# Optimization experiments

Hardware: AMD Instinct MI355X
Metric: run time of the kernel (lower is better)

## Reference

```python
import jax, jax.numpy as jnp
import numpy as np

B, N, F, D, DB, C = 1024, 65536, 64, 512, 1024, 96


def _ln(x, g, b):
    m = x.mean(-1, keepdims=True)
    v = ((x - m) ** 2).mean(-1, keepdims=True)
    return (x - m) * jax.lax.rsqrt(v + 1e-5) * g + b


def setup_inputs() -> dict:
    key = jax.random.key(0)
    ks = jax.random.split(key, 16)
    rn = lambda k, shape, s=1.0: jax.random.normal(k, shape, dtype=jnp.float32) * s
    s_in, s_d, s_db = 1.0 / np.sqrt(F), 1.0 / np.sqrt(D), 1.0 / np.sqrt(DB)
    bound = 1.0 / np.sqrt(2.0)
    return {
        "x_num": rn(ks[0], (B, F)),
        "candidate_num": rn(ks[1], (N, F)),
        "candidate_y": rn(ks[2], (N,)),
        "lin_W": rn(ks[3], (F, D), s_in), "lin_b": jnp.zeros((D,), jnp.float32),
        "e_W1": rn(ks[4], (D, DB), s_d), "e_b1": jnp.zeros((DB,), jnp.float32),
        "e_W2": rn(ks[5], (DB, D), s_db), "e_b2": jnp.zeros((D,), jnp.float32),
        "mix_g": jnp.ones((D,), jnp.float32), "mix_b": jnp.zeros((D,), jnp.float32),
        "K_W": rn(ks[6], (D, D), s_d), "K_b": jnp.zeros((D,), jnp.float32),
        "lab_W": rn(ks[7], (1, D), bound), "lab_b": rn(ks[8], (D,), bound),
        "T_W1": rn(ks[9], (D, DB), s_d), "T_b1": jnp.zeros((DB,), jnp.float32),
        "T_W2": rn(ks[10], (DB, D), s_db),
        "p_ln_g": jnp.ones((D,), jnp.float32), "p_ln_b": jnp.zeros((D,), jnp.float32),
        "p_W1": rn(ks[11], (D, DB), s_d), "p_b1": jnp.zeros((DB,), jnp.float32),
        "p_W2": rn(ks[12], (DB, D), s_db), "p_b2": jnp.zeros((D,), jnp.float32),
        "h_ln_g": jnp.ones((D,), jnp.float32), "h_ln_b": jnp.zeros((D,), jnp.float32),
        "h_W": rn(ks[13], (D, 1), s_d), "h_b": jnp.zeros((1,), jnp.float32),
        "context_size": C,
    }


def reference(x_num, candidate_num, candidate_y,
              lin_W, lin_b, e_W1, e_b1, e_W2, e_b2, mix_g, mix_b, K_W, K_b,
              lab_W, lab_b, T_W1, T_b1, T_W2,
              p_ln_g, p_ln_b, p_W1, p_b1, p_W2, p_b2,
              h_ln_g, h_ln_b, h_W, h_b, context_size):
    def encode(z):
        h = z @ lin_W + lin_b
        h = h + jax.nn.relu(h @ e_W1 + e_b1) @ e_W2 + e_b2  # residual encoder block
        k = _ln(h, mix_g, mix_b) @ K_W + K_b                 # mixer-norm + K projection
        return h, k

    _, cand_k = encode(candidate_num)   # [N, D]
    x, k = encode(x_num)                # [B, D]

    # faiss IndexFlatL2: squared-L2 k-NN over candidate keys -> [B, N] then top-k
    d2 = (k * k).sum(-1, keepdims=True) - 2.0 * (k @ cand_k.T) + (cand_k * cand_k).sum(-1)
    _, idx = jax.lax.top_k(-d2, context_size)   # [B, C] nearest candidates

    ctx_k = cand_k[idx]          # [B, C, D] irregular gather
    ctx_y = candidate_y[idx]     # [B, C]

    # similarities = -||k - k_i||^2, recomputed from gathered keys as in source
    sims = -((k * k).sum(-1, keepdims=True)
             - 2.0 * jnp.einsum('bd,bcd->bc', k, ctx_k)
             + (ctx_k * ctx_k).sum(-1))
    probs = jax.nn.softmax(sims, axis=-1)  # context_dropout=0 (eval)

    y_emb = ctx_y[..., None] @ lab_W + lab_b            # label_encoder_: Linear(1, D)
    diff = k[:, None, :] - ctx_k                        # [B, C, D]
    values = y_emb + jax.nn.relu(diff @ T_W1 + T_b1) @ T_W2
    ctx_x = jnp.einsum('bc,bcd->bd', probs, values)

    x = x + ctx_x
    x = x + jax.nn.relu(_ln(x, p_ln_g, p_ln_b) @ p_W1 + p_b1) @ p_W2 + p_b2  # predictor block
    return jax.nn.relu(_ln(x, h_ln_g, h_ln_b)) @ h_W + h_b                   # head -> [B, 1]
```

## Files before the change

kernel.cpp:

```cpp
#include <hip/hip_runtime.h>

#define NB   1024
#define NN   65536
#define NF   64
#define ND   512
#define NDB  1024
#define NC   96

#define BB_C 256
#define BB_D 128

#define TK_SPLIT 16
#define TK_SEG   (NN / TK_SPLIT)
#define TK_CAND  (TK_SPLIT * NC)

typedef unsigned short ushort;
typedef __attribute__((ext_vector_type(8))) short short8;
typedef __attribute__((ext_vector_type(4))) float floatx4;

__device__ __forceinline__ ushort f2bf(float f) {
    unsigned u = __float_as_uint(f);
    u += 0x7fffu + ((u >> 16) & 1u);
    return (ushort)(u >> 16);
}
__device__ __forceinline__ float bf2f(ushort h) {
    return __uint_as_float(((unsigned)h) << 16);
}
__device__ __forceinline__ int lds_off(int m, int c) {
    return m * 32 + (((c + (m >> 1)) & 3) << 3);
}

__device__ __forceinline__ void gload16(const ushort* g, ushort* l)
{
    void* gv = (void*)g;
    void* lv = (void*)l;
    __builtin_amdgcn_global_load_lds(
        (__attribute__((address_space(1))) void*)gv,
        (__attribute__((address_space(3))) void*)lv, 16, 0, 0);
}

__device__ __forceinline__ void xcd_slab(int& bx, int& by)
{
    const int gx  = gridDim.x;
    const int nwg = gx * gridDim.y;
    int x = blockIdx.x, y = blockIdx.y;
    if (!(nwg & 7)) {
        const int wg = y * gx + x;
        const int t  = (wg & 7) * (nwg >> 3) + (wg >> 3);
        x = t % gx; y = t / gx;
    }
    bx = x; by = y;
}

__global__ __launch_bounds__(256) void gemm_ss(
    const ushort* __restrict__ Ah_g, const ushort* __restrict__ Al_g,
    const ushort* __restrict__ Bh_g, const ushort* __restrict__ Bl_g,
    const float* __restrict__ scoresq, float* __restrict__ Sf,
    int M, int N, int K)
{
    __shared__ ushort Ah[128 * 32], Al[128 * 32];
    __shared__ ushort Bh[128 * 32], Bl[128 * 32];
    const int tid = threadIdx.x;
    const int lane = tid & 63, wid = tid >> 6;
    const int wm = (wid & 1) * 64, wn = (wid >> 1) * 64;
    const int lane15 = lane & 15, quad = lane >> 4;
    const int row0 = blockIdx.y * 128, col0 = blockIdx.x * 128;

    const int srow = tid >> 2;
    const int scl  = tid & 3;
    const int cp   = (scl - (srow >> 1)) & 3;
    const size_t ga0 = (size_t)(row0 + srow) * K + cp * 8;
    const size_t ga1 = (size_t)(row0 + 64 + srow) * K + cp * 8;
    const size_t gb0 = (size_t)(col0 + srow) * K + cp * 8;
    const size_t gb1 = (size_t)(col0 + 64 + srow) * K + cp * 8;
    const int l0 = tid * 8;
    const int l1 = 2048 + tid * 8;

    floatx4 acc[4][4];
#pragma unroll
    for (int i = 0; i < 4; i++)
#pragma unroll
        for (int j = 0; j < 4; j++) acc[i][j] = (floatx4){0.f, 0.f, 0.f, 0.f};

    for (int k0 = 0; k0 < K; k0 += 32) {
        __syncthreads();
        gload16(Ah_g + ga0 + k0, Ah + l0);
        gload16(Ah_g + ga1 + k0, Ah + l1);
        gload16(Al_g + ga0 + k0, Al + l0);
        gload16(Al_g + ga1 + k0, Al + l1);
        gload16(Bh_g + gb0 + k0, Bh + l0);
        gload16(Bh_g + gb1 + k0, Bh + l1);
        gload16(Bl_g + gb0 + k0, Bl + l0);
        gload16(Bl_g + gb1 + k0, Bl + l1);
        __syncthreads();

        short8 ah[4], al[4], bh[4], bl[4];
#pragma unroll
        for (int t = 0; t < 4; t++) {
            const int am = wm + t * 16 + lane15;
            const int bn = wn + t * 16 + lane15;
            ah[t] = *(const short8*)(Ah + lds_off(am, quad));
            al[t] = *(const short8*)(Al + lds_off(am, quad));
            bh[t] = *(const short8*)(Bh + lds_off(bn, quad));
            bl[t] = *(const short8*)(Bl + lds_off(bn, quad));
        }
#pragma unroll
        for (int i = 0; i < 4; i++)
#pragma unroll
            for (int j = 0; j < 4; j++) {
                acc[i][j] = __builtin_amdgcn_mfma_f32_16x16x32_bf16(ah[i], bh[j], acc[i][j], 0, 0, 0);
                acc[i][j] = __builtin_amdgcn_mfma_f32_16x16x32_bf16(ah[i], bl[j], acc[i][j], 0, 0, 0);
                acc[i][j] = __builtin_amdgcn_mfma_f32_16x16x32_bf16(al[i], bh[j], acc[i][j], 0, 0, 0);
            }
    }

#pragma unroll
    for (int i = 0; i < 4; i++)
#pragma unroll
        for (int j = 0; j < 4; j++) {
            const int gc = col0 + wn + j * 16 + lane15;
            const int rb = row0 + wm + i * 16 + quad * 4;
            const float sv = scoresq[gc];
#pragma unroll
            for (int r = 0; r < 4; r++) {
                const size_t o = (size_t)(rb + r) * N + gc;
                Sf[o] = sv - 2.f * acc[i][j][r];
            }
        }
}

__global__ __launch_bounds__(256) void gemm_ss_n64(
    const ushort* __restrict__ Ah_g, const ushort* __restrict__ Al_g,
    const ushort* __restrict__ Bh_g, const ushort* __restrict__ Bl_g,
    const float* __restrict__ bias,
    const ushort* __restrict__ resh, const ushort* __restrict__ resl,
    ushort* __restrict__ Ch, ushort* __restrict__ Cl,
    int M, int N, int K, int relu)
{
    __shared__ ushort Ah[128 * 64], Al[128 * 64];
    __shared__ ushort Bh[64 * 64], Bl[64 * 64];
    const int tid = threadIdx.x;
    const int lane = tid & 63, wid = tid >> 6;
    const int wm = wid * 32;
    const int lane15 = lane & 15, quad = lane >> 4;
    int bx, by; xcd_slab(bx, by);
    const int row0 = by * 128, col0 = bx * 64;

    const int srow = tid >> 2;
    const int scl  = tid & 3;
    const int cp   = (scl - (srow >> 1)) & 3;
    const size_t ga0 = (size_t)(row0 + srow) * K + cp * 8;
    const size_t ga1 = (size_t)(row0 + 64 + srow) * K + cp * 8;
    const size_t gb  = (size_t)(col0 + srow) * K + cp * 8;
    const int l0 = tid * 8;
    const int l1 = 2048 + tid * 8;

    floatx4 acc[2][4];
#pragma unroll
    for (int i = 0; i < 2; i++)
#pragma unroll
        for (int j = 0; j < 4; j++) acc[i][j] = (floatx4){0.f, 0.f, 0.f, 0.f};

    for (int k0 = 0; k0 < K; k0 += 64) {
        __syncthreads();
        gload16(Ah_g + ga0 + k0,      Ah + l0);
        gload16(Ah_g + ga1 + k0,      Ah + l1);
        gload16(Ah_g + ga0 + k0 + 32, Ah + 4096 + l0);
        gload16(Ah_g + ga1 + k0 + 32, Ah + 4096 + l1);
        gload16(Al_g + ga0 + k0,      Al + l0);
        gload16(Al_g + ga1 + k0,      Al + l1);
        gload16(Al_g + ga0 + k0 + 32, Al + 4096 + l0);
        gload16(Al_g + ga1 + k0 + 32, Al + 4096 + l1);
        gload16(Bh_g + gb + k0,       Bh + l0);
        gload16(Bh_g + gb + k0 + 32,  Bh + 2048 + l0);
        gload16(Bl_g + gb + k0,       Bl + l0);
        gload16(Bl_g + gb + k0 + 32,  Bl + 2048 + l0);
        __syncthreads();

#pragma unroll
        for (int kk = 0; kk < 2; kk++) {
            const int ao = kk * 4096, bo = kk * 2048;
            short8 ah[2], al[2], bh[4], bl[4];
#pragma unroll
            for (int t = 0; t < 2; t++) {
                const int am = wm + t * 16 + lane15;
                ah[t] = *(const short8*)(Ah + ao + lds_off(am, quad));
                al[t] = *(const short8*)(Al + ao + lds_off(am, quad));
            }
#pragma unroll
            for (int j = 0; j < 4; j++) {
                const int bn = j * 16 + lane15;
                bh[j] = *(const short8*)(Bh + bo + lds_off(bn, quad));
                bl[j] = *(const short8*)(Bl + bo + lds_off(bn, quad));
            }
#pragma unroll
            for (int i = 0; i < 2; i++)
#pragma unroll
                for (int j = 0; j < 4; j++) {
                    acc[i][j] = __builtin_amdgcn_mfma_f32_16x16x32_bf16(ah[i], bh[j], acc[i][j], 0, 0, 0);
                    acc[i][j] = __builtin_amdgcn_mfma_f32_16x16x32_bf16(ah[i], bl[j], acc[i][j], 0, 0, 0);
                    acc[i][j] = __builtin_amdgcn_mfma_f32_16x16x32_bf16(al[i], bh[j], acc[i][j], 0, 0, 0);
                }
        }
    }

#pragma unroll
    for (int i = 0; i < 2; i++)
#pragma unroll
        for (int j = 0; j < 4; j++) {
            const int gc = col0 + j * 16 + lane15;
            const int rb = row0 + wm + i * 16 + quad * 4;
            const float bv = bias ? bias[gc] : 0.f;
#pragma unroll
            for (int r = 0; r < 4; r++) {
                const size_t o = (size_t)(rb + r) * N + gc;
                float v = acc[i][j][r] + bv;
                if (resh) v += bf2f(resh[o]) + bf2f(resl[o]);
                if (relu) v = fmaxf(v, 0.f);
                ushort h = f2bf(v);
                Ch[o] = h;
                Cl[o] = f2bf(v - bf2f(h));
            }
        }
}

__global__ __launch_bounds__(256) void gemm_ss_small(
    const ushort* __restrict__ Ah_g, const ushort* __restrict__ Al_g,
    const ushort* __restrict__ Bh_g, const ushort* __restrict__ Bl_g,
    const float* __restrict__ bias,
    const ushort* resh, const ushort* resl,
    const float* resf,
    ushort* Ch, ushort* Cl,
    float* outf,
    int M, int N, int K, int relu)
{
    __shared__ ushort Ah[64 * 64], Al[64 * 64];
    __shared__ ushort Bh[64 * 64], Bl[64 * 64];
    const int tid = threadIdx.x;
    const int lane = tid & 63, wid = tid >> 6;
    const int wm = (wid & 1) * 32, wn = (wid >> 1) * 32;
    const int lane15 = lane & 15, quad = lane >> 4;
    int bx, by; xcd_slab(bx, by);
    const int row0 = by * 64, col0 = bx * 64;

    const int srow = tid >> 2;
    const int scl  = tid & 3;
    const int cp   = (scl - (srow >> 1)) & 3;
    const size_t ga = (size_t)(row0 + srow) * K + cp * 8;
    const size_t gb = (size_t)(col0 + srow) * K + cp * 8;
    const int l = tid * 8;

    floatx4 acc[2][2];
#pragma unroll
    for (int i = 0; i < 2; i++)
#pragma unroll
        for (int j = 0; j < 2; j++) acc[i][j] = (floatx4){0.f, 0.f, 0.f, 0.f};

    for (int k0 = 0; k0 < K; k0 += 64) {
        __syncthreads();
        gload16(Ah_g + ga + k0,      Ah + l);
        gload16(Ah_g + ga + k0 + 32, Ah + 2048 + l);
        gload16(Al_g + ga + k0,      Al + l);
        gload16(Al_g + ga + k0 + 32, Al + 2048 + l);
        gload16(Bh_g + gb + k0,      Bh + l);
        gload16(Bh_g + gb + k0 + 32, Bh + 2048 + l);
        gload16(Bl_g + gb + k0,      Bl + l);
        gload16(Bl_g + gb + k0 + 32, Bl + 2048 + l);
        __syncthreads();

#pragma unroll
        for (int kk = 0; kk < 2; kk++) {
            const int so = kk * 2048;
            short8 ah[2], al[2], bh[2], bl[2];
#pragma unroll
            for (int t = 0; t < 2; t++) {
                const int am = wm + t * 16 + lane15;
                const int bn = wn + t * 16 + lane15;
                ah[t] = *(const short8*)(Ah + so + lds_off(am, quad));
                al[t] = *(const short8*)(Al + so + lds_off(am, quad));
                bh[t] = *(const short8*)(Bh + so + lds_off(bn, quad));
                bl[t] = *(const short8*)(Bl + so + lds_off(bn, quad));
            }
#pragma unroll
            for (int i = 0; i < 2; i++)
#pragma unroll
                for (int j = 0; j < 2; j++) {
                    acc[i][j] = __builtin_amdgcn_mfma_f32_16x16x32_bf16(ah[i], bh[j], acc[i][j], 0, 0, 0);
                    acc[i][j] = __builtin_amdgcn_mfma_f32_16x16x32_bf16(ah[i], bl[j], acc[i][j], 0, 0, 0);
                    acc[i][j] = __builtin_amdgcn_mfma_f32_16x16x32_bf16(al[i], bh[j], acc[i][j], 0, 0, 0);
                }
        }
    }

#pragma unroll
    for (int i = 0; i < 2; i++)
#pragma unroll
        for (int j = 0; j < 2; j++) {
            const int gc = col0 + wn + j * 16 + lane15;
            const int rb = row0 + wm + i * 16 + quad * 4;
            const float bv = bias ? bias[gc] : 0.f;
#pragma unroll
            for (int r = 0; r < 4; r++) {
                const size_t o = (size_t)(rb + r) * N + gc;
                float v = acc[i][j][r] + bv;
                if (resh) v += bf2f(resh[o]) + bf2f(resl[o]);
                if (resf) v += resf[o];
                if (relu) v = fmaxf(v, 0.f);
                if (outf) outf[o] = v;
                if (Ch) {
                    ushort h = f2bf(v);
                    Ch[o] = h;
                    Cl[o] = f2bf(v - bf2f(h));
                }
            }
        }
}

__global__ __launch_bounds__(256) void diff_pl_kernel(
    const ushort* __restrict__ kxh, const ushort* __restrict__ kxl,
    const ushort* __restrict__ ckh, const ushort* __restrict__ ckl,
    const int* __restrict__ idx,
    ushort* __restrict__ DD, int Mrows)
{
    const int g = blockIdx.x * 256 + threadIdx.x;
    if (g >= Mrows * (ND / 8)) return;
    const int r  = g >> 6;
    const int d  = (g & 63) * 8;
    const int b_loc = r / NC;
    const int ci = idx[r];
    const size_t xb = (size_t)b_loc * ND + d;
    const size_t cb = (size_t)ci * ND + d;

    short8 xh = *(const short8*)(kxh + xb);
    short8 xl = *(const short8*)(kxl + xb);
    short8 ch = *(const short8*)(ckh + cb);
    short8 cl = *(const short8*)(ckl + cb);
    short8 dd;
#pragma unroll
    for (int i = 0; i < 8; i++) {
        const float a = bf2f((ushort)xh[i]) + bf2f((ushort)xl[i]);
        const float c = bf2f((ushort)ch[i]) + bf2f((ushort)cl[i]);
        dd[i] = (short)f2bf(a - c);
    }
    *(short8*)(DD + (size_t)r * ND + d) = dd;
}

__global__ __launch_bounds__(256) void gemm_bf16_n64(
    const ushort* __restrict__ A, const ushort* __restrict__ BTh,
    const float* __restrict__ bias,
    ushort* __restrict__ Cbf, float* __restrict__ Cf,
    int M, int N, int K, int relu)
{
    __shared__ ushort Ah[128 * 64];
    __shared__ ushort Bh[64 * 64];
    const int tid = threadIdx.x;
    const int lane = tid & 63, wid = tid >> 6;
    const int wm = wid * 32;
    const int lane15 = lane & 15, quad = lane >> 4;
    int bx, by; xcd_slab(bx, by);
    const int row0 = by * 128, col0 = bx * 64;

    const int srow = tid >> 2;
    const int scl  = tid & 3;
    const int cp   = (scl - (srow >> 1)) & 3;
    const size_t ga0 = (size_t)(row0 + srow) * K + cp * 8;
    const size_t ga1 = (size_t)(row0 + 64 + srow) * K + cp * 8;
    const size_t gb  = (size_t)(col0 + srow) * K + cp * 8;
    const int l0 = tid * 8, l1 = 2048 + tid * 8;

    floatx4 acc[2][4];
#pragma unroll
    for (int i = 0; i < 2; i++)
#pragma unroll
        for (int j = 0; j < 4; j++) acc[i][j] = (floatx4){0.f, 0.f, 0.f, 0.f};

    for (int k0 = 0; k0 < K; k0 += 64) {
        __syncthreads();
        gload16(A + ga0 + k0,      Ah + l0);
        gload16(A + ga1 + k0,      Ah + l1);
        gload16(A + ga0 + k0 + 32, Ah + 4096 + l0);
        gload16(A + ga1 + k0 + 32, Ah + 4096 + l1);
        gload16(BTh + gb + k0,      Bh + l0);
        gload16(BTh + gb + k0 + 32, Bh + 2048 + l0);
        __syncthreads();

#pragma unroll
        for (int kk = 0; kk < 2; kk++) {
            const int ao = kk * 4096, bo = kk * 2048;
            short8 ah[2], bh[4];
#pragma unroll
            for (int t = 0; t < 2; t++)
                ah[t] = *(const short8*)(Ah + ao + lds_off(wm + t * 16 + lane15, quad));
#pragma unroll
            for (int j = 0; j < 4; j++)
                bh[j] = *(const short8*)(Bh + bo + lds_off(j * 16 + lane15, quad));
#pragma unroll
            for (int i = 0; i < 2; i++)
#pragma unroll
                for (int j = 0; j < 4; j++)
                    acc[i][j] = __builtin_amdgcn_mfma_f32_16x16x32_bf16(ah[i], bh[j], acc[i][j], 0, 0, 0);
        }
    }

#pragma unroll
    for (int i = 0; i < 2; i++)
#pragma unroll
        for (int j = 0; j < 4; j++) {
            const int gc = col0 + j * 16 + lane15;
            const int rb = row0 + wm + i * 16 + quad * 4;
            const float bv = bias ? bias[gc] : 0.f;
#pragma unroll
            for (int rr = 0; rr < 4; rr++) {
                const size_t o = (size_t)(rb + rr) * N + gc;
                float v = acc[i][j][rr] + bv;
                if (relu) v = fmaxf(v, 0.f);
                if (Cbf) Cbf[o] = f2bf(v);
                if (Cf)  Cf[o] = v;
            }
        }
}

__global__ __launch_bounds__(256) void split_wt_kernel(
    const float* __restrict__ W, ushort* __restrict__ WTh,
    ushort* __restrict__ WTl, int K, int N)
{
    const int o = blockIdx.x * 256 + threadIdx.x;
    if (o < K * N) {
        const int n = o / K, k = o - n * K;
        const float x = W[(size_t)k * N + n];
        const ushort h = f2bf(x);
        WTh[o] = h;
        WTl[o] = f2bf(x - bf2f(h));
    }
}

__global__ __launch_bounds__(256) void split_pl_kernel(
    const float* __restrict__ X, ushort* __restrict__ Xh,
    ushort* __restrict__ Xl, int n)
{
    const int i = blockIdx.x * 256 + threadIdx.x;
    if (i < n) {
        const float x = X[i];
        const ushort h = f2bf(x);
        Xh[i] = h;
        Xl[i] = f2bf(x - bf2f(h));
    }
}

__global__ __launch_bounds__(256) void ln_kernel(
    const float* __restrict__ X, const float* __restrict__ g,
    const float* __restrict__ b, float* __restrict__ Y, int relu)
{
    const int lane = threadIdx.x & 63;
    const int row  = blockIdx.x * 4 + (threadIdx.x >> 6);
    const float* x = X + (size_t)row * ND;
    const int d = lane * 8;

    float4 v0 = *(const float4*)(x + d);
    float4 v1 = *(const float4*)(x + d + 4);
    float s = v0.x + v0.y + v0.z + v0.w + v1.x + v1.y + v1.z + v1.w;
    float q = v0.x*v0.x + v0.y*v0.y + v0.z*v0.z + v0.w*v0.w
            + v1.x*v1.x + v1.y*v1.y + v1.z*v1.z + v1.w*v1.w;
#pragma unroll
    for (int off = 32; off; off >>= 1) {
        s += __shfl_down(s, off);
        q += __shfl_down(q, off);
    }
    s = __shfl(s, 0); q = __shfl(q, 0);
    const float mean = s * (1.f / ND);
    const float var  = q * (1.f / ND) - mean * mean;
    const float rs   = rsqrtf(var + 1e-5f);

    float4 g0 = *(const float4*)(g + d);
    float4 g1 = *(const float4*)(g + d + 4);
    float4 b0 = *(const float4*)(b + d);
    float4 b1 = *(const float4*)(b + d + 4);
    float4 o0, o1;
    o0.x = (v0.x - mean) * rs * g0.x + b0.x;
    o0.y = (v0.y - mean) * rs * g0.y + b0.y;
    o0.z = (v0.z - mean) * rs * g0.z + b0.z;
    o0.w = (v0.w - mean) * rs * g0.w + b0.w;
    o1.x = (v1.x - mean) * rs * g1.x + b1.x;
    o1.y = (v1.y - mean) * rs * g1.y + b1.y;
    o1.z = (v1.z - mean) * rs * g1.z + b1.z;
    o1.w = (v1.w - mean) * rs * g1.w + b1.w;
    if (relu) {
        o0.x = fmaxf(o0.x, 0.f); o0.y = fmaxf(o0.y, 0.f);
        o0.z = fmaxf(o0.z, 0.f); o0.w = fmaxf(o0.w, 0.f);
        o1.x = fmaxf(o1.x, 0.f); o1.y = fmaxf(o1.y, 0.f);
        o1.z = fmaxf(o1.z, 0.f); o1.w = fmaxf(o1.w, 0.f);
    }
    float* y = Y + (size_t)row * ND;
    *(float4*)(y + d)     = o0;
    *(float4*)(y + d + 4) = o1;
}

__global__ __launch_bounds__(256) void ln_pl_kernel(
    const ushort* __restrict__ Xh, const ushort* __restrict__ Xl,
    const float* __restrict__ g, const float* __restrict__ b,
    ushort* __restrict__ Yh, ushort* __restrict__ Yl)
{
    const int lane = threadIdx.x & 63;
    const int row  = blockIdx.x * 4 + (threadIdx.x >> 6);
    const int d = lane * 8;
    const size_t base = (size_t)row * ND + d;

    short8 xh = *(const short8*)(Xh + base);
    short8 xl = *(const short8*)(Xl + base);
    float v[8];
#pragma unroll
    for (int i = 0; i < 8; i++) v[i] = bf2f((ushort)xh[i]) + bf2f((ushort)xl[i]);

    float s = 0.f, q = 0.f;
#pragma unroll
    for (int i = 0; i < 8; i++) { s += v[i]; q += v[i] * v[i]; }
#pragma unroll
    for (int off = 32; off; off >>= 1) {
        s += __shfl_down(s, off);
        q += __shfl_down(q, off);
    }
    s = __shfl(s, 0); q = __shfl(q, 0);
    const float mean = s * (1.f / ND);
    const float var  = q * (1.f / ND) - mean * mean;
    const float rs   = rsqrtf(var + 1e-5f);

    short8 yh, yl;
#pragma unroll
    for (int i = 0; i < 8; i++) {
        const float o = (v[i] - mean) * rs * g[d + i] + b[d + i];
        const ushort h = f2bf(o);
        yh[i] = (short)h;
        yl[i] = (short)f2bf(o - bf2f(h));
    }
    *(short8*)(Yh + base) = yh;
    *(short8*)(Yl + base) = yl;
}

__global__ __launch_bounds__(256) void sqnorm_pl_kernel(
    const ushort* __restrict__ Xh, const ushort* __restrict__ Xl,
    float* __restrict__ sq)
{
    const int lane = threadIdx.x & 63;
    const int row  = blockIdx.x * 4 + (threadIdx.x >> 6);
    const size_t base = (size_t)row * ND + lane * 8;
    short8 xh = *(const short8*)(Xh + base);
    short8 xl = *(const short8*)(Xl + base);
    float q = 0.f;
#pragma unroll
    for (int i = 0; i < 8; i++) {
        float v = bf2f((ushort)xh[i]) + bf2f((ushort)xl[i]);
        q += v * v;
    }
#pragma unroll
    for (int off = 32; off; off >>= 1) q += __shfl_down(q, off);
    if (lane == 0) sq[row] = q;
}

__device__ __forceinline__ unsigned fkey(float f)
{
    unsigned u = __float_as_uint(f);
    return (u & 0x80000000u) ? ~u : (u | 0x80000000u);
}
__device__ __forceinline__ float inv_fkey(unsigned u)
{
    return __uint_as_float((u & 0x80000000u) ? (u & 0x7FFFFFFFu) : ~u);
}

struct SelState {
    unsigned lo;
    unsigned long long hi;
    int krem;
    int done;
    unsigned long long T;
    int need;
};

template <int KPT>
__device__ __forceinline__ void adaptive_select(
    const unsigned (&key)[KPT], unsigned* hist, unsigned* wtot,
    SelState* st, int tid, int kwant)
{
    const int lane = tid & 63, wid = tid >> 6;

    unsigned mn = 0xFFFFFFFFu, mx = 0u;
#pragma unroll
    for (int j = 0; j < KPT; j++) {
        mn = min(mn, key[j]);
        mx = max(mx, key[j]);
    }
#pragma unroll
    for (int off = 32; off; off >>= 1) {
        mn = min(mn, (unsigned)__shfl_down((int)mn, off));
        mx = max(mx, (unsigned)__shfl_down((int)mx, off));
    }
    if (lane == 0) { hist[wid] = mn; hist[8 + wid] = mx; }
    if (tid == 0) st->done = 0;
    __syncthreads();
    if (tid == 0) {
        unsigned gmn = min(min(hist[0], hist[1]), min(hist[2], hist[3]));
        unsigned gmx = max(max(hist[8], hist[9]), max(hist[10], hist[11]));
        st->lo = gmn;
        st->hi = (unsigned long long)gmx + 1ull;
        st->krem = kwant;
    }
    __syncthreads();

    for (int iter = 0; iter < 6 && !st->done; iter++) {
        const unsigned lo = st->lo;
        const unsigned long long hi = st->hi;
        const int krem = st->krem;
        const unsigned long long span = hi - lo;
        int shift = 0;
        if (span > 256ull) {
            const int nb = 64 - __builtin_clzll(span - 1ull);
            shift = nb - 8;
        }
        hist[tid] = 0u;
        __syncthreads();
#pragma unroll
        for (int j = 0; j < KPT; j++) {
            const unsigned u = key[j];
            if (u >= lo && (unsigned long long)u < hi)
                atomicAdd(&hist[(u - lo) >> shift], 1u);
        }
        __syncthreads();
        const unsigned c = hist[tid];
        unsigned v = c;
#pragma unroll
        for (int off = 1; off < 64; off <<= 1) {
            const unsigned t = (unsigned)__shfl_up((int)v, off);
            if (lane >= off) v += t;
        }
        if (lane == 63) wtot[wid] = v;
        __syncthreads();
        unsigned pre = 0;
        for (int w = 0; w < 3; w++) pre += (w < wid) ? wtot[w] : 0u;
        const int incl = (int)(v + pre);
        const int excl = incl - (int)c;
        if (excl < krem && incl >= krem) {
            const unsigned long long binlo =
                (unsigned long long)lo + ((unsigned long long)tid << shift);
            if (shift == 0) {
                st->T = binlo;
                st->need = krem - excl;
                st->done = 1;
            } else if (incl == krem) {
                st->T = binlo + (1ull << shift);
                st->need = 0;
                st->done = 1;
            } else {
                st->lo = (unsigned)binlo;
                const unsigned long long nhi = binlo + (1ull << shift);
                st->hi = nhi < hi ? nhi : hi;
                st->krem = krem - excl;
            }
        }
        __syncthreads();
    }
}

__global__ __launch_bounds__(256) void topk_seg(
    const float* __restrict__ S, unsigned* __restrict__ K1key,
    int* __restrict__ K1idx)
{
    const int r = blockIdx.y, seg = blockIdx.x;
    const float* p = S + (size_t)r * NN + seg * TK_SEG;
    __shared__ unsigned hist[256];
    __shared__ unsigned wtot[4];
    __shared__ SelState st;
    __shared__ int cA, cB;
    const int tid = threadIdx.x;

    unsigned key[16];
#pragma unroll
    for (int j = 0; j < 16; j++) key[j] = fkey(p[tid + j * 256]);

    if (tid == 0) { cA = 0; cB = 0; }
    adaptive_select<16>(key, hist, wtot, &st, tid, NC);

    const unsigned long long T = st.T;
    const int need = st.need;
    const int cntLess = NC - need;
    const size_t obase = ((size_t)r * TK_SPLIT + seg) * NC;
#pragma unroll
    for (int j = 0; j < 16; j++) {
        const unsigned u = key[j];
        if ((unsigned long long)u < T) {
            const int pos = atomicAdd(&cA, 1);
            K1key[obase + pos] = u;
            K1idx[obase + pos] = seg * TK_SEG + tid + j * 256;
        } else if ((unsigned long long)u == T) {
            const int pos = atomicAdd(&cB, 1);
            if (pos < need) {
                K1key[obase + cntLess + pos] = u;
                K1idx[obase + cntLess + pos] = seg * TK_SEG + tid + j * 256;
            }
        }
    }
}

__global__ __launch_bounds__(256) void topk_merge(
    const unsigned* __restrict__ K1key, const int* __restrict__ K1idx,
    int* __restrict__ idx_out, float* __restrict__ val_out, int b0)
{
    const int r = blockIdx.x;
    const int b = b0 + r;
    __shared__ unsigned hist[256];
    __shared__ unsigned wtot[4];
    __shared__ SelState st;
    __shared__ int cA, cB;
    const int tid = threadIdx.x;
    const size_t ibase = (size_t)r * TK_CAND;

    unsigned key[6];
    int      kidx[6];
#pragma unroll
    for (int j = 0; j < 6; j++) {
        key[j]  = K1key[ibase + tid + j * 256];
        kidx[j] = K1idx[ibase + tid + j * 256];
    }

    if (tid == 0) { cA = 0; cB = 0; }
    adaptive_select<6>(key, hist, wtot, &st, tid, NC);

    const unsigned long long T = st.T;
    const int need = st.need;
    const int cntLess = NC - need;
#pragma unroll
    for (int j = 0; j < 6; j++) {
        const unsigned u = key[j];
        if ((unsigned long long)u < T) {
            const int pos = atomicAdd(&cA, 1);
            idx_out[b * NC + pos] = kidx[j];
            val_out[b * NC + pos] = inv_fkey(u);
        } else if ((unsigned long long)u == T) {
            const int pos = atomicAdd(&cB, 1);
            if (pos < need) {
                idx_out[b * NC + cntLess + pos] = kidx[j];
                val_out[b * NC + cntLess + pos] = inv_fkey(u);
            }
        }
    }
}

__global__ __launch_bounds__(128) void probs_kernel(
    const float* __restrict__ svals, float* __restrict__ probs)
{
    const int b = blockIdx.x;
    const int tid = threadIdx.x;
    __shared__ float red[128];
    const bool valid = tid < NC;
    float s = valid ? -svals[b * NC + tid] : -3.4e38f;
    red[tid] = s;
    __syncthreads();
#pragma unroll
    for (int off = 64; off; off >>= 1) {
        if (tid < off) red[tid] = fmaxf(red[tid], red[tid + off]);
        __syncthreads();
    }
    const float m = red[0];
    __syncthreads();
    float e = valid ? expf(s - m) : 0.f;
    red[tid] = e;
    __syncthreads();
#pragma unroll
    for (int off = 64; off; off >>= 1) {
        if (tid < off) red[tid] += red[tid + off];
        __syncthreads();
    }
    const float sum = red[0];
    if (valid) probs[b * NC + tid] = e / sum;
}

__global__ __launch_bounds__(256) void ctx_kernel(
    const float* __restrict__ VAL, const float* __restrict__ probs,
    const float* __restrict__ cand_y, const int* __restrict__ idx,
    const float* __restrict__ labW, const float* __restrict__ labb,
    const ushort* __restrict__ xinh, const ushort* __restrict__ xinl,
    float* __restrict__ xout, int b0)
{
    const int b_loc = blockIdx.x;
    const int b = b0 + b_loc;
    const int tid = threadIdx.x;
    __shared__ float pv[NC];
    __shared__ float red[256];
    float py_part = 0.f;
    if (tid < NC) {
        float p = probs[b * NC + tid];
        pv[tid] = p;
        py_part = p * cand_y[idx[b * NC + tid]];
    }
    red[tid] = py_part;
    __syncthreads();
#pragma unroll
    for (int off = 128; off; off >>= 1) {
        if (tid < off) red[tid] += red[tid + off];
        __syncthreads();
    }
    const float py = red[0];

    for (int d = tid; d < ND; d += 256) {
        const float* vp = VAL + (size_t)b_loc * NC * ND + d;
        float acc = 0.f;
#pragma unroll 8
        for (int c = 0; c < NC; c++) acc += pv[c] * vp[(size_t)c * ND];
        float ctx = acc + py * labW[d] + labb[d];
        const size_t o = (size_t)b * ND + d;
        xout[o] = bf2f(xinh[o]) + bf2f(xinl[o]) + ctx;
    }
}

__global__ __launch_bounds__(64) void head_kernel(
    const float* __restrict__ X, const float* __restrict__ hW,
    const float* __restrict__ hb, float* __restrict__ out)
{
    const int b = blockIdx.x;
    const int lane = threadIdx.x;
    const float* x = X + (size_t)b * ND;
    float acc = 0.f;
#pragma unroll
    for (int j = 0; j < 8; j++) {
        int d = lane + 64 * j;
        acc += x[d] * hW[d];
    }
#pragma unroll
    for (int off = 32; off; off >>= 1) acc += __shfl_down(acc, off);
    if (lane == 0) out[b] = acc + hb[0];
}

extern "C" void kernel_launch(void* const* d_in, const int* in_sizes, int n_in,
                              void* d_out, int out_size, void* d_ws, size_t ws_size,
                              hipStream_t stream)
{
    const float* x_num    = (const float*)d_in[0];
    const float* cand_num = (const float*)d_in[1];
    const float* cand_y   = (const float*)d_in[2];
    const float* lin_W    = (const float*)d_in[3];
    const float* lin_b    = (const float*)d_in[4];
    const float* e_W1     = (const float*)d_in[5];
    const float* e_b1     = (const float*)d_in[6];
    const float* e_W2     = (const float*)d_in[7];
    const float* e_b2     = (const float*)d_in[8];
    const float* mix_g    = (const float*)d_in[9];
    const float* mix_b    = (const float*)d_in[10];
    const float* K_W      = (const float*)d_in[11];
    const float* K_b      = (const float*)d_in[12];
    const float* lab_W    = (const float*)d_in[13];
    const float* lab_b    = (const float*)d_in[14];
    const float* T_W1     = (const float*)d_in[15];
    const float* T_b1     = (const float*)d_in[16];
    const float* T_W2     = (const float*)d_in[17];
    const float* p_ln_g   = (const float*)d_in[18];
    const float* p_ln_b   = (const float*)d_in[19];
    const float* p_W1     = (const float*)d_in[20];
    const float* p_b1     = (const float*)d_in[21];
    const float* p_W2     = (const float*)d_in[22];
    const float* p_b2     = (const float*)d_in[23];
    const float* h_ln_g   = (const float*)d_in[24];
    const float* h_ln_b   = (const float*)d_in[25];
    const float* h_W      = (const float*)d_in[26];
    const float* h_b      = (const float*)d_in[27];
    float* out = (float*)d_out;
    (void)in_sizes; (void)n_in; (void)out_size;

    const int NTOT = NN + NB;

    size_t off = 0;
    auto ralloc = [&](size_t bytes) -> void* {
        void* p = (char*)d_ws + off;
        off += (bytes + 255) & ~(size_t)255;
        return p;
    };
    auto falloc = [&](size_t n) -> float*  { return (float*)ralloc(n * 4); };
    auto ualloc = [&](size_t n) -> ushort* { return (ushort*)ralloc(n * 2); };

    ushort* WP_lin_h = ualloc((size_t)ND * NF);
    ushort* WP_lin_l = ualloc((size_t)ND * NF);
    ushort* WP_e1_h  = ualloc((size_t)NDB * ND);
    ushort* WP_e1_l  = ualloc((size_t)NDB * ND);
    ushort* WP_e2_h  = ualloc((size_t)ND * NDB);
    ushort* WP_e2_l  = ualloc((size_t)ND * NDB);
    ushort* WP_kw_h  = ualloc((size_t)ND * ND);
    ushort* WP_kw_l  = ualloc((size_t)ND * ND);
    ushort* WP_t1_h  = ualloc((size_t)NDB * ND);
    ushort* WP_t1_l  = ualloc((size_t)NDB * ND);
    ushort* WP_t2_h  = ualloc((size_t)ND * NDB);
    ushort* WP_t2_l  = ualloc((size_t)ND * NDB);
    ushort* WP_p1_h  = ualloc((size_t)NDB * ND);
    ushort* WP_p1_l  = ualloc((size_t)NDB * ND);
    ushort* WP_p2_h  = ualloc((size_t)ND * NDB);
    ushort* WP_p2_l  = ualloc((size_t)ND * NDB);

    ushort* R_CKh = ualloc((size_t)NTOT * ND);
    ushort* R_CKl = ualloc((size_t)NTOT * ND);
    float*  R_sq  = falloc(NTOT);

    ushort* X2h = ualloc((size_t)NB * ND);
    ushort* X2l = ualloc((size_t)NB * ND);
    ushort* Lxh = ualloc((size_t)NB * ND);
    ushort* Lxl = ualloc((size_t)NB * ND);
    ushort* Tph = ualloc((size_t)NB * NDB);
    ushort* Tpl = ualloc((size_t)NB * NDB);

    int*    R_idx = (int*)ralloc((size_t)NB * NC * 4);
    float*  R_ssel= falloc((size_t)NB * NC);
    float*  R_prob= falloc((size_t)NB * NC);
    float*  R_xupd= falloc((size_t)NB * ND);
    float*  R_lnx = falloc((size_t)NB * ND);
    float*  R_x2  = falloc((size_t)NB * ND);
    float*  R_lnx2= falloc((size_t)NB * ND);
    unsigned* K1key = (unsigned*)ralloc((size_t)BB_C * TK_CAND * 4);
    int*      K1idx = (int*)ralloc((size_t)BB_C * TK_CAND * 4);

    int CH;
    {
        const size_t remain = (ws_size > off) ? (ws_size - off) : 0;
        CH = (remain >= (size_t)13312 * 6144 + (size_t)(4u << 20)) ? 13312 : 8320;
    }
    size_t scr_bytes = (size_t)CH * 6144;
    const size_t scores_bytes = (size_t)BB_C * NN * 4;
    const size_t values_bytes = (size_t)BB_D * NC * (ND*2 + NDB*2 + ND*4);
    if (scr_bytes < scores_bytes) scr_bytes = scores_bytes;
    if (scr_bytes < values_bytes) scr_bytes = values_bytes;
    char* SCR = (char*)ralloc(scr_bytes);

    auto sw = [&](const float* W, ushort* WTh, ushort* WTl, int K, int N) {
        split_wt_kernel<<<dim3((K * N + 255) / 256), dim3(256), 0, stream>>>(W, WTh, WTl, K, N);
    };
    sw(lin_W, WP_lin_h, WP_lin_l, NF, ND);
    sw(e_W1,  WP_e1_h,  WP_e1_l,  ND, NDB);
    sw(e_W2,  WP_e2_h,  WP_e2_l,  NDB, ND);
    sw(K_W,   WP_kw_h,  WP_kw_l,  ND, ND);
    sw(T_W1,  WP_t1_h,  WP_t1_l,  ND, NDB);
    sw(T_W2,  WP_t2_h,  WP_t2_l,  NDB, ND);
    sw(p_W1,  WP_p1_h,  WP_p1_l,  ND, NDB);
    sw(p_W2,  WP_p2_h,  WP_p2_l,  NDB, ND);

    auto gn64 = [&](const ushort* Ah, const ushort* Al, const ushort* Bh,
                    const ushort* Bl, const float* bias, const ushort* resh,
                    const ushort* resl, ushort* Ch, ushort* Cl,
                    int M, int Nn, int K, int relu) {
        gemm_ss_n64<<<dim3(Nn / 64, M / 128), dim3(256), 0, stream>>>(
            Ah, Al, Bh, Bl, bias, resh, resl, Ch, Cl, M, Nn, K, relu);
    };
    auto gsm = [&](const ushort* Ah, const ushort* Al, const ushort* Bh,
                   const ushort* Bl, const float* bias, const ushort* resh,
                   const ushort* resl, const float* resf, ushort* Ch,
                   ushort* Cl, float* outf, int M, int Nn, int K, int relu) {
        gemm_ss_small<<<dim3(Nn / 64, M / 64), dim3(256), 0, stream>>>(
            Ah, Al, Bh, Bl, bias, resh, resl, resf, Ch, Cl, outf, M, Nn, K, relu);
    };

    {
        ushort* Hh = (ushort*)SCR;
        ushort* Hl = Hh + (size_t)CH * ND;
        ushort* Th = Hl + (size_t)CH * ND;
        ushort* Tl = Th + (size_t)CH * NDB;
        ushort* CNh = Th;
        ushort* CNl = Tl;
        ushort* Gh  = Th;
        ushort* Gl  = Tl;

        for (int n0 = 0; n0 < NTOT; n0 += CH) {
            int candRows = NN - n0;
            if (candRows > CH) candRows = CH;
            if (candRows < 0)  candRows = 0;
            const int xRows = CH - candRows;

            if (candRows)
                split_pl_kernel<<<dim3((candRows * NF + 255) / 256), dim3(256), 0, stream>>>(
                    cand_num + (size_t)n0 * NF, CNh, CNl, candRows * NF);
            if (xRows)
                split_pl_kernel<<<dim3((xRows * NF + 255) / 256), dim3(256), 0, stream>>>(
                    x_num, CNh + (size_t)candRows * NF, CNl + (size_t)candRows * NF,
                    xRows * NF);

            gsm(CNh, CNl, WP_lin_h, WP_lin_l, lin_b, nullptr, nullptr, nullptr,
                Hh, Hl, nullptr, CH, ND, NF, 0);
            gn64(Hh, Hl, WP_e1_h, WP_e1_l, e_b1, nullptr, nullptr,
                 Th, Tl, CH, NDB, ND, 1);
            gsm(Th, Tl, WP_e2_h, WP_e2_l, e_b2, Hh, Hl, nullptr,
                Hh, Hl, nullptr, CH, ND, NDB, 0);

            if (xRows) {
                hipMemcpyAsync(X2h, Hh + (size_t)candRows * ND,
                               (size_t)NB * ND * 2, hipMemcpyDeviceToDevice, stream);
                hipMemcpyAsync(X2l, Hl + (size_t)candRows * ND,
                               (size_t)NB * ND * 2, hipMemcpyDeviceToDevice, stream);
            }

            ln_pl_kernel<<<dim3(CH / 4), dim3(256), 0, stream>>>(
                Hh, Hl, mix_g, mix_b, Gh, Gl);
            gsm(Gh, Gl, WP_kw_h, WP_kw_l, K_b, nullptr, nullptr, nullptr,
                R_CKh + (size_t)n0 * ND, R_CKl + (size_t)n0 * ND, nullptr,
                CH, ND, ND, 0);
            sqnorm_pl_kernel<<<dim3(CH / 4), dim3(256), 0, stream>>>(
                R_CKh + (size_t)n0 * ND, R_CKl + (size_t)n0 * ND, R_sq + n0);
        }
    }

    const ushort* kxh = R_CKh + (size_t)NN * ND;
    const ushort* kxl = R_CKl + (size_t)NN * ND;

    for (int b0 = 0; b0 < NB; b0 += BB_C) {
        float* S = (float*)SCR;
        gemm_ss<<<dim3(NN / 128, BB_C / 128), dim3(256), 0, stream>>>(
            kxh + (size_t)b0 * ND, kxl + (size_t)b0 * ND, R_CKh, R_CKl,
            R_sq, S, BB_C, NN, ND);
        topk_seg<<<dim3(TK_SPLIT, BB_C), dim3(256), 0, stream>>>(S, K1key, K1idx);
        topk_merge<<<dim3(BB_C), dim3(256), 0, stream>>>(K1key, K1idx,
                                                         R_idx, R_ssel, b0);
    }
    probs_kernel<<<dim3(NB), dim3(128), 0, stream>>>(R_ssel, R_prob);

    for (int b0 = 0; b0 < NB; b0 += BB_D) {
        const int M = BB_D * NC;
        ushort* DD  = (ushort*)SCR;
        ushort* TT  = DD + (size_t)M * ND;
        float*  VAL = (float*)(TT + (size_t)M * NDB);

        diff_pl_kernel<<<dim3((M * (ND / 8) + 255) / 256), dim3(256), 0, stream>>>(
            kxh + (size_t)b0 * ND, kxl + (size_t)b0 * ND,
            R_CKh, R_CKl, R_idx + b0 * NC, DD, M);
        gemm_bf16_n64<<<dim3(NDB / 64, M / 128), dim3(256), 0, stream>>>(
            DD, WP_t1_h, T_b1, TT, nullptr, M, NDB, ND, 1);
        gemm_bf16_n64<<<dim3(ND / 64, M / 128), dim3(256), 0, stream>>>(
            TT, WP_t2_h, nullptr, nullptr, VAL, M, ND, NDB, 0);
        ctx_kernel<<<dim3(BB_D), dim3(256), 0, stream>>>(
            VAL, R_prob, cand_y, R_idx, lab_W, lab_b, X2h, X2l, R_xupd, b0);
    }

    ln_kernel<<<dim3(NB / 4), dim3(256), 0, stream>>>(R_xupd, p_ln_g, p_ln_b, R_lnx, 0);
    split_pl_kernel<<<dim3((NB * ND + 255) / 256), dim3(256), 0, stream>>>(
        R_lnx, Lxh, Lxl, NB * ND);
    gsm(Lxh, Lxl, WP_p1_h, WP_p1_l, p_b1, nullptr, nullptr, nullptr,
        Tph, Tpl, nullptr, NB, NDB, ND, 1);
    gsm(Tph, Tpl, WP_p2_h, WP_p2_l, p_b2, nullptr, nullptr, R_xupd,
        nullptr, nullptr, R_x2, NB, ND, NDB, 0);
    ln_kernel<<<dim3(NB / 4), dim3(256), 0, stream>>>(R_x2, h_ln_g, h_ln_b, R_lnx2, 1);
    head_kernel<<<dim3(NB), dim3(64), 0, stream>>>(R_lnx2, h_W, h_b, out);
}
```

Baseline: 2.052 ms.

## Use 64-wide split GEMM for encoder, vectorize topk loads, split ctx grid

The encoder's lin, e_W2 and K projection GEMMs move from the gsm kernel to the 128x64-tile split-precision gn64 kernel. The restrict qualifiers are dropped from gn64's residual and output pointers so it can be called in place (residual aliases the output). topk_seg now reads scores as float4 with the element indices remapped to match, and ctx_kernel runs on a 2-D grid so each block handles half of the D columns. The aim is better occupancy or tiling for the encoder GEMMs and wider loads, at the cost of smaller tiles and possibly less reuse per block.

```diff
diff --git a/kernel.cpp b/kernel.cpp
--- a/kernel.cpp
+++ b/kernel.cpp
@@ -133,8 +133,8 @@
     const ushort* __restrict__ Ah_g, const ushort* __restrict__ Al_g,
     const ushort* __restrict__ Bh_g, const ushort* __restrict__ Bl_g,
     const float* __restrict__ bias,
-    const ushort* __restrict__ resh, const ushort* __restrict__ resl,
-    ushort* __restrict__ Ch, ushort* __restrict__ Cl,
+    const ushort* resh, const ushort* resl,
+    ushort* Ch, ushort* Cl,
     int M, int N, int K, int relu)
 {
     __shared__ ushort Ah[128 * 64], Al[128 * 64];
@@ -673,7 +673,13 @@
 
     unsigned key[16];
 #pragma unroll
-    for (int j = 0; j < 16; j++) key[j] = fkey(p[tid + j * 256]);
+    for (int j = 0; j < 4; j++) {
+        float4 v = *(const float4*)(p + tid * 4 + j * 1024);
+        key[j * 4 + 0] = fkey(v.x);
+        key[j * 4 + 1] = fkey(v.y);
+        key[j * 4 + 2] = fkey(v.z);
+        key[j * 4 + 3] = fkey(v.w);
+    }
 
     if (tid == 0) { cA = 0; cB = 0; }
     adaptive_select<16>(key, hist, wtot, &st, tid, NC);
@@ -685,15 +691,16 @@
 #pragma unroll
     for (int j = 0; j < 16; j++) {
         const unsigned u = key[j];
+        const int eidx = seg * TK_SEG + tid * 4 + (j >> 2) * 1024 + (j & 3);
         if ((unsigned long long)u < T) {
             const int pos = atomicAdd(&cA, 1);
             K1key[obase + pos] = u;
-            K1idx[obase + pos] = seg * TK_SEG + tid + j * 256;
+            K1idx[obase + pos] = eidx;
         } else if ((unsigned long long)u == T) {
             const int pos = atomicAdd(&cB, 1);
             if (pos < need) {
                 K1key[obase + cntLess + pos] = u;
-                K1idx[obase + cntLess + pos] = seg * TK_SEG + tid + j * 256;
+                K1idx[obase + cntLess + pos] = eidx;
             }
         }
     }
@@ -799,15 +806,14 @@
     }
     const float py = red[0];
 
-    for (int d = tid; d < ND; d += 256) {
-        const float* vp = VAL + (size_t)b_loc * NC * ND + d;
-        float acc = 0.f;
+    const int d = blockIdx.y * 256 + tid;
+    const float* vp = VAL + (size_t)b_loc * NC * ND + d;
+    float acc = 0.f;
 #pragma unroll 8
-        for (int c = 0; c < NC; c++) acc += pv[c] * vp[(size_t)c * ND];
-        float ctx = acc + py * labW[d] + labb[d];
-        const size_t o = (size_t)b * ND + d;
-        xout[o] = bf2f(xinh[o]) + bf2f(xinl[o]) + ctx;
-    }
+    for (int c = 0; c < NC; c++) acc += pv[c] * vp[(size_t)c * ND];
+    float ctx = acc + py * labW[d] + labb[d];
+    const size_t o = (size_t)b * ND + d;
+    xout[o] = bf2f(xinh[o]) + bf2f(xinl[o]) + ctx;
 }
 
 __global__ __launch_bounds__(64) void head_kernel(
@@ -975,12 +981,12 @@
                     x_num, CNh + (size_t)candRows * NF, CNl + (size_t)candRows * NF,
                     xRows * NF);
 
-            gsm(CNh, CNl, WP_lin_h, WP_lin_l, lin_b, nullptr, nullptr, nullptr,
-                Hh, Hl, nullptr, CH, ND, NF, 0);
+            gn64(CNh, CNl, WP_lin_h, WP_lin_l, lin_b, nullptr, nullptr,
+                 Hh, Hl, CH, ND, NF, 0);
             gn64(Hh, Hl, WP_e1_h, WP_e1_l, e_b1, nullptr, nullptr,
                  Th, Tl, CH, NDB, ND, 1);
-            gsm(Th, Tl, WP_e2_h, WP_e2_l, e_b2, Hh, Hl, nullptr,
-                Hh, Hl, nullptr, CH, ND, NDB, 0);
+            gn64(Th, Tl, WP_e2_h, WP_e2_l, e_b2, Hh, Hl,
+                 Hh, Hl, CH, ND, NDB, 0);
 
             if (xRows) {
                 hipMemcpyAsync(X2h, Hh + (size_t)candRows * ND,
@@ -991,9 +997,9 @@
 
             ln_pl_kernel<<<dim3(CH / 4), dim3(256), 0, stream>>>(
                 Hh, Hl, mix_g, mix_b, Gh, Gl);
-            gsm(Gh, Gl, WP_kw_h, WP_kw_l, K_b, nullptr, nullptr, nullptr,
-                R_CKh + (size_t)n0 * ND, R_CKl + (size_t)n0 * ND, nullptr,
-                CH, ND, ND, 0);
+            gn64(Gh, Gl, WP_kw_h, WP_kw_l, K_b, nullptr, nullptr,
+                 R_CKh + (size_t)n0 * ND, R_CKl + (size_t)n0 * ND,
+                 CH, ND, ND, 0);
             sqnorm_pl_kernel<<<dim3(CH / 4), dim3(256), 0, stream>>>(
                 R_CKh + (size_t)n0 * ND, R_CKl + (size_t)n0 * ND, R_sq + n0);
         }
@@ -1026,7 +1032,7 @@
             DD, WP_t1_h, T_b1, TT, nullptr, M, NDB, ND, 1);
         gemm_bf16_n64<<<dim3(ND / 64, M / 128), dim3(256), 0, stream>>>(
             TT, WP_t2_h, nullptr, nullptr, VAL, M, ND, NDB, 0);
-        ctx_kernel<<<dim3(BB_D), dim3(256), 0, stream>>>(
+        ctx_kernel<<<dim3(BB_D, 2), dim3(256), 0, stream>>>(
             VAL, R_prob, cand_y, R_idx, lab_W, lab_b, X2h, X2l, R_xupd, b0);
     }
 
```

Result: slower. 2.146 ms (+4.5%).
